# Optimization experiments

Hardware: AMD Instinct MI355X
Metric: run time of the kernel (lower is better)

Reference implementation:

```python
import jax, jax.numpy as jnp
import numpy as np

HID = 2048; S = 2048; NH = 16
Q_LORA = 1536; KV_LORA = 512
D_NOPE = 128; D_ROPE = 64; D_V = 128
D_QK = D_NOPE + D_ROPE  # 192
EPS = 1e-6


def setup_inputs() -> dict:
    key = jax.random.key(0)
    ks = jax.random.split(key, 8)
    hidden_states = jax.random.normal(ks[0], (1, S, HID), dtype=jnp.float32)
    # real RoPE tables, HF layout: cos/sin = concat(freqs, freqs) along last dim
    inv_freq = 1.0 / (10000.0 ** (np.arange(0, D_ROPE, 2, dtype=np.float32) / D_ROPE))
    t = np.arange(S, dtype=np.float32)
    freqs = np.outer(t, inv_freq)  # [S, D_ROPE//2]
    emb = np.concatenate([freqs, freqs], axis=-1)  # [S, D_ROPE]
    cos = jnp.asarray(np.cos(emb))[None]  # [1, S, D_ROPE]
    sin = jnp.asarray(np.sin(emb))[None]
    def lin(k, fan_in, fan_out):
        return jax.random.normal(k, (fan_in, fan_out), dtype=jnp.float32) / np.sqrt(fan_in)
    return {
        'hidden_states': hidden_states, 'cos': cos, 'sin': sin,
        'w_qa': lin(ks[1], HID, Q_LORA),
        'g_qa': jnp.ones((Q_LORA,), jnp.float32),
        'w_qb': lin(ks[2], Q_LORA, NH * D_QK),
        'w_kva': lin(ks[3], HID, KV_LORA + D_ROPE),
        'g_kva': jnp.ones((KV_LORA,), jnp.float32),
        'w_kvb': lin(ks[4], KV_LORA, NH * (D_NOPE + D_V)),
        'w_o': lin(ks[5], NH * D_V, HID),
    }


def _rmsnorm(x, g):
    var = jnp.mean(x * x, axis=-1, keepdims=True)
    return x * jax.lax.rsqrt(var + EPS) * g


def _deinterleave(x):
    # view (..., d//2, 2) -> transpose -> reshape: even-index dims first, then odd
    b, h, s, d = x.shape
    return x.reshape(b, h, s, d // 2, 2).transpose(0, 1, 2, 4, 3).reshape(b, h, s, d)


def _rotate_half(x):
    x1, x2 = jnp.split(x, 2, axis=-1)
    return jnp.concatenate([-x2, x1], axis=-1)


def _apply_rope(q, k, cos, sin):
    cos = cos[:, None]  # [B,1,S,D]
    sin = sin[:, None]
    q = _deinterleave(q)
    k = _deinterleave(k)
    q_emb = q * cos + _rotate_half(q) * sin
    k_emb = k * cos + _rotate_half(k) * sin
    return q_emb, k_emb


def reference(hidden_states, cos, sin, w_qa, g_qa, w_qb, w_kva, g_kva, w_kvb, w_o):
    bsz, q_len, _ = hidden_states.shape
    # low-rank Q projection
    q = _rmsnorm(hidden_states @ w_qa, g_qa) @ w_qb  # [B,S,NH*D_QK]
    q = q.reshape(bsz, q_len, NH, D_QK).transpose(0, 2, 1, 3)  # [B,NH,S,D_QK]
    q_nope, q_pe = q[..., :D_NOPE], q[..., D_NOPE:]
    # compressed KV + shared rope key
    ckv = hidden_states @ w_kva  # [B,S,KV_LORA+D_ROPE]
    compressed_kv, k_pe = ckv[..., :KV_LORA], ckv[..., KV_LORA:]
    k_pe = k_pe.reshape(bsz, q_len, 1, D_ROPE).transpose(0, 2, 1, 3)  # [B,1,S,D_ROPE]
    kv = (_rmsnorm(compressed_kv, g_kva) @ w_kvb).reshape(bsz, q_len, NH, D_NOPE + D_V).transpose(0, 2, 1, 3)
    k_nope, value_states = kv[..., :D_NOPE], kv[..., D_NOPE:]
    # interleaved RoPE
    q_pe, k_pe = _apply_rope(q_pe, k_pe, cos, sin)
    query_states = jnp.concatenate([q_nope, q_pe], axis=-1)  # [B,NH,S,D_QK]
    key_states = jnp.concatenate([k_nope, jnp.broadcast_to(k_pe, (bsz, NH, q_len, D_ROPE))], axis=-1)
    # causal attention with MLA softmax scale
    scale = D_QK ** (-0.5)
    scores = jnp.einsum('bhqd,bhkd->bhqk', query_states, key_states) * scale
    mask = jnp.tril(jnp.ones((q_len, q_len), dtype=bool))
    scores = jnp.where(mask, scores, jnp.finfo(scores.dtype).min)
    probs = jax.nn.softmax(scores, axis=-1)
    attn = jnp.einsum('bhqk,bhkd->bhqd', probs, value_states)  # [B,NH,S,D_V]
    attn = attn.transpose(0, 2, 1, 3).reshape(bsz, q_len, NH * D_V)
    return attn @ w_o
```

## Files before the change

### kernel.cpp

```cpp
#include <hip/hip_runtime.h>
#include <hip/hip_bf16.h>

#define S_LEN 2048
#define HID_D 2048
#define NHEAD 16
#define QLORA 1536
#define KVLORA 512
#define DNOPE 128
#define DROPE 64
#define DV 128
#define DQK 192
#define CKV_PAD 640

#define KS_SH (64 * 192)
#define VS_SH (128 * 64)
#define BUF_SH (KS_SH + VS_SH)

typedef __hip_bfloat16 bf16;
typedef __attribute__((ext_vector_type(8))) short short8;
typedef __attribute__((ext_vector_type(4))) short s16x4;
typedef __attribute__((ext_vector_type(4))) float f32x4;

__device__ __forceinline__ float ldE(const float* p) { return *p; }
__device__ __forceinline__ float ldE(const bf16* p) { return __bfloat162float(*p); }
__device__ __forceinline__ void stE(float* p, float v) { *p = v; }
__device__ __forceinline__ void stE(bf16* p, float v) { *p = __float2bfloat16(v); }

__device__ __forceinline__ short bf16bits(float v) {
    __hip_bfloat16 h = __float2bfloat16(v);
    return *reinterpret_cast<short*>(&h);
}

__device__ __forceinline__ float b2f(short s) {
    union { short s; bf16 h; } u;
    u.s = s;
    return __bfloat162float(u.h);
}

__device__ __forceinline__ f32x4 mfma16(short8 a, short8 b, f32x4 c) {
    return __builtin_amdgcn_mfma_f32_16x16x32_bf16(a, b, c, 0, 0, 0);
}

__device__ __forceinline__ void gload16(const void* g, void* l) {
    __builtin_amdgcn_global_load_lds(
        (const __attribute__((address_space(1))) unsigned int*)g,
        (__attribute__((address_space(3))) unsigned int*)l, 16, 0, 0);
}

__global__ void detect_kernel(const void* hidden, int* flag) {
    __shared__ int red[256];
    const int tid = threadIdx.x;
    const bf16* hb = (const bf16*)hidden;
    float a = fabsf(__bfloat162float(hb[tid]));
    red[tid] = (!(a < 64.f) || (a != 0.f && a < 1e-30f)) ? 1 : 0;
    __syncthreads();
    for (int o = 128; o > 0; o >>= 1) {
        if (tid < o) red[tid] += red[tid + o];
        __syncthreads();
    }
    if (tid == 0) *flag = (red[0] > 16) ? 1 : 0;
}

__global__ void convert_kernel(const void* in, bf16* out, int n8, const int* flag) {
    int i = blockIdx.x * 256 + threadIdx.x;
    if (i >= n8) return;
    size_t off = (size_t)i * 8;
    short8 o;
    if (*flag) {
        const float* f = (const float*)in + off;
#pragma unroll
        for (int j = 0; j < 8; ++j) o[j] = bf16bits(f[j]);
    } else {
        o = *(const short8*)((const short*)in + off);
    }
    *(short8*)((short*)out + off) = o;
}

__global__ void transpose_kernel(const void* in, bf16* out, int K, int N, int Npad,
                                 const int* flag) {
    __shared__ __align__(16) short Ts[64][80];
    const int tid = threadIdx.x;
    const int n0 = blockIdx.x * 64, k0 = blockIdx.y * 64;
    const bool inb = n0 < N;
    const int fp32 = *flag;
    const int kl = tid >> 4;
    const int nl = (tid & 15) * 4;
#pragma unroll
    for (int p = 0; p < 4; ++p) {
        int k = kl + p * 16;
        float v[4] = {0.f, 0.f, 0.f, 0.f};
        if (inb) {
            if (fp32) {
                const float4 f = *(const float4*)((const float*)in + (size_t)(k0 + k) * N + n0 + nl);
                v[0] = f.x; v[1] = f.y; v[2] = f.z; v[3] = f.w;
            } else {
                const bf16* bp = (const bf16*)in + (size_t)(k0 + k) * N + n0 + nl;
#pragma unroll
                for (int i = 0; i < 4; ++i) v[i] = __bfloat162float(bp[i]);
            }
        }
#pragma unroll
        for (int i = 0; i < 4; ++i) Ts[nl + i][k] = bf16bits(v[i]);
    }
    __syncthreads();
    const int nr = tid >> 2;
    const int kq = (tid & 3) * 16;
    short* op = (short*)out + (size_t)(n0 + nr) * K + k0 + kq;
    *(short8*)op = *(short8*)&Ts[nr][kq];
    *(short8*)(op + 8) = *(short8*)&Ts[nr][kq + 8];
}

template <int MODE, typename TC>
__device__ void mgemm_body(const bf16* __restrict__ A, const bf16* __restrict__ Bt,
                           TC* __restrict__ C, int M, int N, int K,
                           bf16* __restrict__ Kn, bf16* __restrict__ Vt) {
    __shared__ __align__(16) short As[128 * 32];
    __shared__ __align__(16) short Bs[128 * 32];
    const int tid = threadIdx.x;
    const int w = tid >> 6, lane = tid & 63;
    const int lg = lane >> 4, ln = lane & 15;
    const int wm = w >> 1, wn = w & 1;
    const int m0 = blockIdx.y * 128, n0 = blockIdx.x * 128;

    const int c0 = w * 128 + lane, c1 = c0 + 64;
    const int r0 = c0 >> 2, kq0 = (c0 & 3) ^ ((r0 >> 1) & 3);
    const int r1 = c1 >> 2, kq1 = (c1 & 3) ^ ((r1 >> 1) & 3);
    const bf16* aP0 = A + (size_t)(m0 + r0) * K + kq0 * 8;
    const bf16* aP1 = A + (size_t)(m0 + r1) * K + kq1 * 8;
    const bf16* bP0 = Bt + (size_t)(n0 + r0) * K + kq0 * 8;
    const bf16* bP1 = Bt + (size_t)(n0 + r1) * K + kq1 * 8;
    short* aL0 = As + (size_t)(w * 128) * 8;
    short* aL1 = As + (size_t)(w * 128 + 64) * 8;
    short* bL0 = Bs + (size_t)(w * 128) * 8;
    short* bL1 = Bs + (size_t)(w * 128 + 64) * 8;

    const int sx = lg ^ ((ln >> 1) & 3);
    int aoff[4], boff[4];
#pragma unroll
    for (int i = 0; i < 4; ++i) {
        aoff[i] = (wm * 64 + i * 16 + ln) * 32 + sx * 8;
        boff[i] = (wn * 64 + i * 16 + ln) * 32 + sx * 8;
    }

    f32x4 acc[4][4];
#pragma unroll
    for (int i = 0; i < 4; ++i)
#pragma unroll
        for (int j = 0; j < 4; ++j) acc[i][j] = (f32x4){0.f, 0.f, 0.f, 0.f};

    for (int k0 = 0; k0 < K; k0 += 32) {
        __syncthreads();
        gload16(aP0 + k0, aL0);
        gload16(aP1 + k0, aL1);
        gload16(bP0 + k0, bL0);
        gload16(bP1 + k0, bL1);
        __syncthreads();
        short8 af[4], bfr[4];
#pragma unroll
        for (int i = 0; i < 4; ++i) af[i] = *(const short8*)&As[aoff[i]];
#pragma unroll
        for (int j = 0; j < 4; ++j) bfr[j] = *(const short8*)&Bs[boff[j]];
#pragma unroll
        for (int i = 0; i < 4; ++i)
#pragma unroll
            for (int j = 0; j < 4; ++j) acc[i][j] = mfma16(af[i], bfr[j], acc[i][j]);
    }
    if constexpr (MODE == 2) {
#pragma unroll
        for (int i = 0; i < 4; ++i)
#pragma unroll
            for (int j = 0; j < 4; ++j) {
                const int col = n0 + wn * 64 + j * 16 + ln;
                const int row = m0 + wm * 64 + i * 16 + lg * 4;
                const int h = col >> 8, d = col & 255;
                if (d < DNOPE) {
                    bf16* cp = Kn + (size_t)row * (NHEAD * DNOPE) + h * DNOPE + d;
#pragma unroll
                    for (int r = 0; r < 4; ++r)
                        cp[(size_t)r * (NHEAD * DNOPE)] = __float2bfloat16(acc[i][j][r]);
                } else {
                    s16x4 pk;
#pragma unroll
                    for (int r = 0; r < 4; ++r) pk[r] = bf16bits(acc[i][j][r]);
                    *(s16x4*)(Vt + (size_t)(h * DV + (d - DNOPE)) * S_LEN + row) = pk;
                }
            }
    } else {
#pragma unroll
        for (int i = 0; i < 4; ++i)
#pragma unroll
            for (int j = 0; j < 4; ++j) {
                TC* cp = C + (size_t)(m0 + wm * 64 + i * 16 + lg * 4) * N + n0 + wn * 64 + j * 16 + ln;
#pragma unroll
                for (int r = 0; r < 4; ++r)
                    stE(cp + (size_t)r * N, acc[i][j][r]);
            }
    }
}

template <int MODE>
__global__ __launch_bounds__(256, 2)
void mgemm_kernel(const bf16* A, const bf16* Bt, void* C, int M, int N, int K,
                  const int* flag, bf16* Kn, bf16* Vt) {
    if (MODE == 1 && *flag) mgemm_body<1, float>(A, Bt, (float*)C, M, N, K, nullptr, nullptr);
    else if (MODE == 2)     mgemm_body<2, bf16>(A, Bt, (bf16*)C, M, N, K, Kn, Vt);
    else                    mgemm_body<0, bf16>(A, Bt, (bf16*)C, M, N, K, nullptr, nullptr);
}

template <typename TG>
__device__ void rmsnorm_body(const bf16* __restrict__ x, const TG* __restrict__ g,
                             bf16* __restrict__ y, int len, int xstride, int ystride) {
    const int s = blockIdx.x;
    const int tid = threadIdx.x;
    const bf16* xr = x + (size_t)s * xstride;
    float ss = 0.f;
    for (int i = tid; i < len; i += 256) {
        float v = __bfloat162float(xr[i]);
        ss += v * v;
    }
    __shared__ float red[256];
    red[tid] = ss;
    __syncthreads();
    for (int o = 128; o > 0; o >>= 1) {
        if (tid < o) red[tid] += red[tid + o];
        __syncthreads();
    }
    const float scale = rsqrtf(red[0] / (float)len + 1e-6f);
    bf16* yr = y + (size_t)s * ystride;
    for (int i = tid; i < len; i += 256)
        yr[i] = __float2bfloat16(__bfloat162float(xr[i]) * scale * ldE(&g[i]));
}

__global__ void rmsnorm_kernel(const bf16* x, const void* g, bf16* y,
                               int len, int xstride, int ystride, const int* flag) {
    if (*flag) rmsnorm_body<float>(x, (const float*)g, y, len, xstride, ystride);
    else       rmsnorm_body<bf16>(x, (const bf16*)g, y, len, xstride, ystride);
}

template <typename TG>
__device__ void rope_body(bf16* __restrict__ q, const bf16* __restrict__ ckv,
                          bf16* __restrict__ kpe, const TG* __restrict__ cosb,
                          const TG* __restrict__ sinb) {
    const int s = blockIdx.x;
    const int tid = threadIdx.x;
    float x0 = 0.f, x1 = 0.f, c = 0.f, sn = 0.f;
    bf16* qbase = nullptr;
    int p = 0;
    const bool isq = tid < 512;
    const bool active = tid < 544;
    if (active) {
        if (isq) {
            const int h = tid >> 5;
            p = tid & 31;
            qbase = q + (size_t)s * (NHEAD * DQK) + h * DQK + DNOPE;
            x0 = __bfloat162float(qbase[2 * p]);
            x1 = __bfloat162float(qbase[2 * p + 1]);
        } else {
            p = tid - 512;
            const bf16* kb = ckv + (size_t)s * CKV_PAD + KVLORA;
            x0 = __bfloat162float(kb[2 * p]);
            x1 = __bfloat162float(kb[2 * p + 1]);
        }
        c = ldE(&cosb[s * 64 + p]);
        sn = ldE(&sinb[s * 64 + p]);
    }
    __syncthreads();
    if (active) {
        if (isq) {
            qbase[p] = __float2bfloat16(x0 * c - x1 * sn);
            qbase[p + 32] = __float2bfloat16(x1 * c + x0 * sn);
        } else {
            kpe[s * 64 + p] = __float2bfloat16(x0 * c - x1 * sn);
            kpe[s * 64 + p + 32] = __float2bfloat16(x1 * c + x0 * sn);
        }
    }
}

__global__ void rope_kernel(bf16* q, const bf16* ckv, bf16* kpe,
                            const void* cosb, const void* sinb, const int* flag) {
    if (*flag) rope_body<float>(q, ckv, kpe, (const float*)cosb, (const float*)sinb);
    else       rope_body<bf16>(q, ckv, kpe, (const bf16*)cosb, (const bf16*)sinb);
}

__global__ __launch_bounds__(256, 2)
void fattn_kernel(const bf16* __restrict__ q, const bf16* __restrict__ kn,
                  const bf16* __restrict__ vt, const bf16* __restrict__ kpe,
                  bf16* __restrict__ attn, bf16* __restrict__ Opart, float* __restrict__ ml) {
    const int nf = blockIdx.x;
    const int xcd = nf & 7;
    const int j = nf >> 3;
    const int bx = j & 31;
    const int h = (j >> 5) * 8 + xcd;
    int qt, part, nparts;
    if (bx < 15)      { qt = 15 - bx / 3;        part = bx % 3;        nparts = 3; }
    else if (bx < 27) { qt = 10 - (bx - 15) / 2; part = (bx - 15) & 1; nparts = 2; }
    else              { qt = 31 - bx;            part = 0;             nparts = 1; }
    const int nt = 2 * qt + 2;
    const int bsz = nt / nparts, rr = nt % nparts;
    const int t0 = part * bsz + (part < rr ? part : rr);
    const int t1 = t0 + bsz + (part < rr ? 1 : 0);
    const int q0 = qt * 128;

    const int tid = threadIdx.x;
    const int w = tid >> 6;
    const int l = tid & 63;
    const int lg = l >> 4;
    const int ln = l & 15;

    __shared__ __align__(16) short KV[2][BUF_SH];

    int offK[6], sK[6];
    bool isn[6];
#pragma unroll
    for (int p = 0; p < 6; ++p) {
        const int cid = tid + p * 256;
        const int row = cid / 24;
        const int cpos = cid % 24;
        const int c = (cpos & 24) | ((cpos & 7) ^ (row & 7));
        if (c < 16) {
            offK[p] = row * (NHEAD * DNOPE) + h * DNOPE + c * 8;
            sK[p] = NHEAD * DNOPE;
            isn[p] = true;
        } else {
            offK[p] = row * DROPE + (c - 16) * 8;
            sK[p] = DROPE;
            isn[p] = false;
        }
    }
    int offV[4];
#pragma unroll
    for (int p = 0; p < 4; ++p) {
        const int cid = tid + p * 256;
        const int row = cid >> 3;
        const int cc = (cid & 7) ^ (row & 7);
        offV[p] = (h * DV + row) * S_LEN + cc * 8;
    }

    short8 qf[2][6];
#pragma unroll
    for (int i = 0; i < 2; ++i) {
        const short* qrow =
            (const short*)(q + (size_t)(q0 + i * 64 + w * 16 + ln) * (NHEAD * DQK) + h * DQK);
#pragma unroll
        for (int ks = 0; ks < 6; ++ks)
            qf[i][ks] = *(const short8*)(qrow + ks * 32 + lg * 8);
    }

    f32x4 O[2][8];
#pragma unroll
    for (int i = 0; i < 2; ++i)
#pragma unroll
        for (int ct = 0; ct < 8; ++ct) O[i][ct] = (f32x4){0.f, 0.f, 0.f, 0.f};
    float m_[2][4], l_[2][4];
#pragma unroll
    for (int i = 0; i < 2; ++i)
#pragma unroll
        for (int r = 0; r < 4; ++r) { m_[i][r] = -1e30f; l_[i][r] = 0.f; }
    const float scale = 0.07216878364870322f;

    {
        const int k0 = t0 * 64;
#pragma unroll
        for (int p = 0; p < 6; ++p) {
            const bf16* sp = (isn[p] ? kn : kpe) + (size_t)offK[p] + (size_t)k0 * sK[p];
            gload16(sp, &KV[0][0] + (w + 4 * p) * 512);
        }
#pragma unroll
        for (int p = 0; p < 4; ++p)
            gload16(vt + (size_t)offV[p] + k0, &KV[0][KS_SH] + (w + 4 * p) * 512);
    }

    for (int t = t0; t < t1; ++t) {
        const int cur = (t - t0) & 1;
        short* Ks = &KV[cur][0];
        short* Vs = &KV[cur][KS_SH];
        if (t + 1 < t1) {
            const int k0n = (t + 1) * 64;
            short* KsN = &KV[cur ^ 1][0];
            short* VsN = &KV[cur ^ 1][KS_SH];
#pragma unroll
            for (int p = 0; p < 6; ++p) {
                const bf16* sp = (isn[p] ? kn : kpe) + (size_t)offK[p] + (size_t)k0n * sK[p];
                gload16(sp, KsN + (w + 4 * p) * 512);
            }
#pragma unroll
            for (int p = 0; p < 4; ++p)
                gload16(vt + (size_t)offV[p] + k0n, VsN + (w + 4 * p) * 512);
            asm volatile("s_waitcnt vmcnt(10)" ::: "memory");
        } else {
            asm volatile("s_waitcnt vmcnt(0)" ::: "memory");
        }
        __builtin_amdgcn_s_barrier();

        const int k0 = t * 64;
        f32x4 S[2][4];
#pragma unroll
        for (int i = 0; i < 2; ++i)
#pragma unroll
            for (int c = 0; c < 4; ++c) S[i][c] = (f32x4){0.f, 0.f, 0.f, 0.f};
        __builtin_amdgcn_s_setprio(1);
#pragma unroll
        for (int ks = 0; ks < 6; ++ks) {
            const int kch = ks * 4 + lg;
#pragma unroll
            for (int c = 0; c < 4; ++c) {
                short8 kf = *(const short8*)&Ks[(size_t)(c * 16 + ln) * 192 +
                                               (size_t)(kch ^ (ln & 7)) * 8];
                S[0][c] = mfma16(qf[0][ks], kf, S[0][c]);
                S[1][c] = mfma16(qf[1][ks], kf, S[1][c]);
            }
        }
        __builtin_amdgcn_s_setprio(0);

        const int d0 = k0 - q0;
#pragma unroll
        for (int i = 0; i < 2; ++i)
#pragma unroll
            for (int c = 0; c < 4; ++c)
#pragma unroll
                for (int r = 0; r < 4; ++r) {
                    float v = S[i][c][r] * scale;
                    if (d0 > -64 &&
                        (d0 + c * 16 + ln) > (i * 64 + w * 16 + lg * 4 + r)) v = -1e30f;
                    S[i][c][r] = v;
                }

        float alpha[2][4];
#pragma unroll
        for (int i = 0; i < 2; ++i)
#pragma unroll
            for (int r = 0; r < 4; ++r) {
                float mx = fmaxf(fmaxf(S[i][0][r], S[i][1][r]), fmaxf(S[i][2][r], S[i][3][r]));
#pragma unroll
                for (int d = 1; d < 16; d <<= 1) mx = fmaxf(mx, __shfl_xor(mx, d));
                float mn = fmaxf(m_[i][r], mx);
                alpha[i][r] = __expf(m_[i][r] - mn);
                m_[i][r] = mn;
                float rs = 0.f;
#pragma unroll
                for (int c = 0; c < 4; ++c) {
                    float p = __expf(S[i][c][r] - mn);
                    S[i][c][r] = p;
                    rs += p;
                }
#pragma unroll
                for (int d = 1; d < 16; d <<= 1) rs += __shfl_xor(rs, d);
                l_[i][r] = l_[i][r] * alpha[i][r] + rs;
            }
#pragma unroll
        for (int i = 0; i < 2; ++i)
#pragma unroll
            for (int ct = 0; ct < 8; ++ct)
#pragma unroll
                for (int r = 0; r < 4; ++r) O[i][ct][r] *= alpha[i][r];

        __builtin_amdgcn_s_barrier();
        short* Pb = Ks;
#pragma unroll
        for (int i = 0; i < 2; ++i)
#pragma unroll
            for (int c = 0; c < 4; ++c)
#pragma unroll
                for (int r = 0; r < 4; ++r)
                    Pb[(size_t)(i * 64 + w * 16 + lg * 4 + r) * 70 + c * 16 + ln] =
                        bf16bits(S[i][c][r]);

        __builtin_amdgcn_s_setprio(1);
#pragma unroll
        for (int ks = 0; ks < 2; ++ks) {
            short8 pf0 = *(const short8*)&Pb[(size_t)(w * 16 + ln) * 70 + ks * 32 + lg * 8];
            short8 pf1 = *(const short8*)&Pb[(size_t)(64 + w * 16 + ln) * 70 + ks * 32 + lg * 8];
#pragma unroll
            for (int ct = 0; ct < 8; ++ct) {
                short8 vf = *(const short8*)&Vs[(size_t)(ct * 16 + ln) * 64 +
                                               (size_t)((ks * 4 + lg) ^ (ln & 7)) * 8];
                O[0][ct] = mfma16(pf0, vf, O[0][ct]);
                O[1][ct] = mfma16(pf1, vf, O[1][ct]);
            }
        }
        __builtin_amdgcn_s_setprio(0);
        __builtin_amdgcn_s_barrier();
    }

    if (nparts == 1) {
#pragma unroll
        for (int i = 0; i < 2; ++i)
#pragma unroll
            for (int r = 0; r < 4; ++r) {
                float inv = 1.f / l_[i][r];
                bf16* orow = attn + (size_t)(q0 + i * 64 + w * 16 + lg * 4 + r) * (NHEAD * DV) +
                             h * DV;
#pragma unroll
                for (int ct = 0; ct < 8; ++ct)
                    orow[ct * 16 + ln] = __float2bfloat16(O[i][ct][r] * inv);
            }
    } else {
        const int mlslot = h * 27 + (qt <= 10 ? (qt - 5) * 2 + part : 12 + (qt - 11) * 3 + part);
        float* mlp = ml + (size_t)mlslot * 128 * 2;
        if (part == 0) {
#pragma unroll
            for (int i = 0; i < 2; ++i)
#pragma unroll
                for (int r = 0; r < 4; ++r) {
                    const int rowb = i * 64 + w * 16 + lg * 4 + r;
                    bf16* orow = attn + (size_t)(q0 + rowb) * (NHEAD * DV) + h * DV;
#pragma unroll
                    for (int ct = 0; ct < 8; ++ct)
                        orow[ct * 16 + ln] = __float2bfloat16(O[i][ct][r]);
                    if (ln == 0) {
                        mlp[rowb * 2] = m_[i][r];
                        mlp[rowb * 2 + 1] = l_[i][r];
                    }
                }
        } else {
            const int oslot = h * 16 + (qt <= 10 ? (qt - 5) : 6 + (qt - 11) * 2 + (part - 1));
            bf16* op = Opart + (size_t)oslot * 128 * DV;
#pragma unroll
            for (int i = 0; i < 2; ++i)
#pragma unroll
                for (int r = 0; r < 4; ++r) {
                    const int rowb = i * 64 + w * 16 + lg * 4 + r;
#pragma unroll
                    for (int ct = 0; ct < 8; ++ct)
                        op[(size_t)rowb * DV + ct * 16 + ln] = __float2bfloat16(O[i][ct][r]);
                    if (ln == 0) {
                        mlp[rowb * 2] = m_[i][r];
                        mlp[rowb * 2 + 1] = l_[i][r];
                    }
                }
        }
    }
}

__global__ void reduce_kernel(const bf16* __restrict__ Opart, const float* __restrict__ ml,
                              bf16* __restrict__ attn) {
    const int qq = blockIdx.x;
    const int h = blockIdx.y;
    const int qt = 5 + qq;
    const int np = (qt <= 10) ? 2 : 3;
    const int q0 = qt * 128;
    const int tid = threadIdx.x;
    const int row = tid >> 1;
    const int dh = (tid & 1) * 64;
    float mp[3], lp[3], f[3];
    float mm = -1e30f;
    for (int p = 0; p < np; ++p) {
        const int msl = h * 27 + (qt <= 10 ? (qt - 5) * 2 + p : 12 + (qt - 11) * 3 + p);
        mp[p] = ml[((size_t)msl * 128 + row) * 2];
        lp[p] = ml[((size_t)msl * 128 + row) * 2 + 1];
        mm = fmaxf(mm, mp[p]);
    }
    float denom = 0.f;
    for (int p = 0; p < np; ++p) {
        f[p] = __expf(mp[p] - mm);
        denom += f[p] * lp[p];
    }
    const float inv = 1.f / denom;
    const int os1 = h * 16 + (qt <= 10 ? (qt - 5) : 6 + (qt - 11) * 2);
    bf16* arow = attn + (size_t)(q0 + row) * (NHEAD * DV) + h * DV + dh;
    const bf16* o1 = Opart + ((size_t)os1 * 128 + row) * DV + dh;
    const bf16* o2 = o1 + (size_t)128 * DV;
#pragma unroll
    for (int jc = 0; jc < 8; ++jc) {
        short8 a = *(const short8*)(arow + jc * 8);
        short8 b1 = *(const short8*)(o1 + jc * 8);
        short8 b2 = (np == 3) ? *(const short8*)(o2 + jc * 8) : b1;
        short8 o;
#pragma unroll
        for (int e = 0; e < 8; ++e) {
            float v = f[0] * b2f(a[e]) + f[1] * b2f(b1[e]);
            if (np == 3) v += f[2] * b2f(b2[e]);
            o[e] = bf16bits(v * inv);
        }
        *(short8*)(arow + jc * 8) = o;
    }
}

extern "C" void kernel_launch(void* const* d_in, const int* in_sizes, int n_in,
                              void* d_out, int out_size, void* d_ws, size_t ws_size,
                              hipStream_t stream) {
    const void* hidden = d_in[0];
    const void* cosb   = d_in[1];
    const void* sinb   = d_in[2];
    const void* w_qa   = d_in[3];
    const void* g_qa   = d_in[4];
    const void* w_qb   = d_in[5];
    const void* w_kva  = d_in[6];
    const void* g_kva  = d_in[7];
    const void* w_kvb  = d_in[8];
    const void* w_o    = d_in[9];

    bf16* ws = (bf16*)d_ws;
    bf16* q_a  = ws;
    bf16* ckv  = q_a + (size_t)S_LEN * QLORA;
    bf16* ckvn = ckv + (size_t)S_LEN * CKV_PAD;
    bf16* q    = ckvn + (size_t)S_LEN * KVLORA;
    bf16* kn   = q + (size_t)S_LEN * NHEAD * DQK;
    bf16* vtb  = kn + (size_t)S_LEN * NHEAD * DNOPE;
    bf16* kpe  = vtb + (size_t)NHEAD * DV * S_LEN;
    bf16* hbf  = kpe + (size_t)S_LEN * DROPE;
    int* flag  = (int*)(hbf + (size_t)S_LEN * HID_D);
    bf16* attn = ws;
    float* ml  = (float*)(ws + (size_t)S_LEN * HID_D);
    bf16* Opart = hbf;
    bf16* W01  = kn;
    bf16* W23  = q_a;
    bf16* W4   = q;

    detect_kernel<<<1, 256, 0, stream>>>(hidden, flag);
    convert_kernel<<<(S_LEN * HID_D / 8 + 255) / 256, 256, 0, stream>>>(
        hidden, hbf, S_LEN * HID_D / 8, flag);

    transpose_kernel<<<dim3(QLORA / 64, HID_D / 64), 256, 0, stream>>>(
        w_qa, W01, HID_D, QLORA, QLORA, flag);
    mgemm_kernel<0><<<dim3(QLORA / 128, S_LEN / 128), 256, 0, stream>>>(
        hbf, W01, q_a, S_LEN, QLORA, HID_D, flag, nullptr, nullptr);
    rmsnorm_kernel<<<S_LEN, 256, 0, stream>>>(q_a, g_qa, q_a, QLORA, QLORA, QLORA, flag);
    transpose_kernel<<<dim3(NHEAD * DQK / 64, QLORA / 64), 256, 0, stream>>>(
        w_qb, W01, QLORA, NHEAD * DQK, NHEAD * DQK, flag);
    mgemm_kernel<0><<<dim3(NHEAD * DQK / 128, S_LEN / 128), 256, 0, stream>>>(
        q_a, W01, q, S_LEN, NHEAD * DQK, QLORA, flag, nullptr, nullptr);
    transpose_kernel<<<dim3(CKV_PAD / 64, HID_D / 64), 256, 0, stream>>>(
        w_kva, W23, HID_D, KVLORA + DROPE, CKV_PAD, flag);
    mgemm_kernel<0><<<dim3(CKV_PAD / 128, S_LEN / 128), 256, 0, stream>>>(
        hbf, W23, ckv, S_LEN, CKV_PAD, HID_D, flag, nullptr, nullptr);
    rmsnorm_kernel<<<S_LEN, 256, 0, stream>>>(ckv, g_kva, ckvn, KVLORA, CKV_PAD, KVLORA, flag);
    transpose_kernel<<<dim3(NHEAD * (DNOPE + DV) / 64, KVLORA / 64), 256, 0, stream>>>(
        w_kvb, W23, KVLORA, NHEAD * (DNOPE + DV), NHEAD * (DNOPE + DV), flag);
    mgemm_kernel<2><<<dim3(NHEAD * (DNOPE + DV) / 128, S_LEN / 128), 256, 0, stream>>>(
        ckvn, W23, kn, S_LEN, NHEAD * (DNOPE + DV), KVLORA, flag, kn, vtb);
    rope_kernel<<<S_LEN, 576, 0, stream>>>(q, ckv, kpe, cosb, sinb, flag);
    fattn_kernel<<<dim3(512), 256, 0, stream>>>(q, kn, vtb, kpe, attn, Opart, ml);
    reduce_kernel<<<dim3(11, NHEAD), 256, 0, stream>>>(Opart, ml, attn);
    transpose_kernel<<<dim3(HID_D / 64, HID_D / 64), 256, 0, stream>>>(
        w_o, W4, HID_D, HID_D, HID_D, flag);
    mgemm_kernel<1><<<dim3(HID_D / 128, S_LEN / 128), 256, 0, stream>>>(
        attn, W4, d_out, S_LEN, HID_D, HID_D, flag, nullptr, nullptr);
}
```

Before: 408.4 us.

## Merge q_a and kv_a projections into one GEMM and deepen GEMM K-tile

Concatenates the transposed w_qa and w_kva weights so a single GEMM over the hidden states produces both the q low-rank and compressed-KV outputs, with fused transpose and RMSNorm launches for both branches. The GEMM gains explicit leading dimensions and a K step of 64 instead of 32, with an 8-way XOR swizzle, halving the number of barrier pairs per tile. This removes several launches and the CKV padding and improves per-barrier MFMA density. In exchange LDS use per block doubles, which may limit occupancy, and workspace aliasing becomes more intricate.

```diff
diff --git a/kernel.cpp b/kernel.cpp
--- a/kernel.cpp
+++ b/kernel.cpp
@@ -10,7 +10,7 @@
 #define DROPE 64
 #define DV 128
 #define DQK 192
-#define CKV_PAD 640
+#define NCAT 2176
 
 #define KS_SH (64 * 192)
 #define VS_SH (128 * 64)
@@ -76,6 +76,39 @@
     *(short8*)((short*)out + off) = o;
 }
 
+template <int KDIM>
+__device__ void transpose_tile(const void* in, bf16* out, int N, int n0, int k0,
+                               int roff, int fp32) {
+    __shared__ __align__(16) short Ts[64][80];
+    const int tid = threadIdx.x;
+    const bool inb = n0 < N;
+    const int kl = tid >> 4;
+    const int nl = (tid & 15) * 4;
+#pragma unroll
+    for (int p = 0; p < 4; ++p) {
+        int k = kl + p * 16;
+        float v[4] = {0.f, 0.f, 0.f, 0.f};
+        if (inb) {
+            if (fp32) {
+                const float4 f = *(const float4*)((const float*)in + (size_t)(k0 + k) * N + n0 + nl);
+                v[0] = f.x; v[1] = f.y; v[2] = f.z; v[3] = f.w;
+            } else {
+                const bf16* bp = (const bf16*)in + (size_t)(k0 + k) * N + n0 + nl;
+#pragma unroll
+                for (int i = 0; i < 4; ++i) v[i] = __bfloat162float(bp[i]);
+            }
+        }
+#pragma unroll
+        for (int i = 0; i < 4; ++i) Ts[nl + i][k] = bf16bits(v[i]);
+    }
+    __syncthreads();
+    const int nr = tid >> 2;
+    const int kq = (tid & 3) * 16;
+    short* op = (short*)out + (size_t)(roff + n0 + nr) * KDIM + k0 + kq;
+    *(short8*)op = *(short8*)&Ts[nr][kq];
+    *(short8*)(op + 8) = *(short8*)&Ts[nr][kq + 8];
+}
+
 __global__ void transpose_kernel(const void* in, bf16* out, int K, int N, int Npad,
                                  const int* flag) {
     __shared__ __align__(16) short Ts[64][80];
@@ -110,37 +143,48 @@
     *(short8*)(op + 8) = *(short8*)&Ts[nr][kq + 8];
 }
 
+__global__ void transpose2_kernel(const void* inA, const void* inB, bf16* out,
+                                  const int* flag) {
+    const int bx = blockIdx.x;
+    const int k0 = blockIdx.y * 64;
+    const int fp32 = *flag;
+    if (bx < 24) transpose_tile<HID_D>(inA, out, QLORA, bx * 64, k0, 0, fp32);
+    else         transpose_tile<HID_D>(inB, out, KVLORA + DROPE, (bx - 24) * 64, k0, QLORA, fp32);
+}
+
 template <int MODE, typename TC>
-__device__ void mgemm_body(const bf16* __restrict__ A, const bf16* __restrict__ Bt,
-                           TC* __restrict__ C, int M, int N, int K,
+__device__ void mgemm_body(const bf16* __restrict__ A, int lda,
+                           const bf16* __restrict__ Bt, int ldb,
+                           TC* __restrict__ C, int ldc, int K,
                            bf16* __restrict__ Kn, bf16* __restrict__ Vt) {
-    __shared__ __align__(16) short As[128 * 32];
-    __shared__ __align__(16) short Bs[128 * 32];
+    __shared__ __align__(16) short As[128 * 64];
+    __shared__ __align__(16) short Bs[128 * 64];
     const int tid = threadIdx.x;
     const int w = tid >> 6, lane = tid & 63;
     const int lg = lane >> 4, ln = lane & 15;
     const int wm = w >> 1, wn = w & 1;
     const int m0 = blockIdx.y * 128, n0 = blockIdx.x * 128;
 
-    const int c0 = w * 128 + lane, c1 = c0 + 64;
-    const int r0 = c0 >> 2, kq0 = (c0 & 3) ^ ((r0 >> 1) & 3);
-    const int r1 = c1 >> 2, kq1 = (c1 & 3) ^ ((r1 >> 1) & 3);
-    const bf16* aP0 = A + (size_t)(m0 + r0) * K + kq0 * 8;
-    const bf16* aP1 = A + (size_t)(m0 + r1) * K + kq1 * 8;
-    const bf16* bP0 = Bt + (size_t)(n0 + r0) * K + kq0 * 8;
-    const bf16* bP1 = Bt + (size_t)(n0 + r1) * K + kq1 * 8;
-    short* aL0 = As + (size_t)(w * 128) * 8;
-    short* aL1 = As + (size_t)(w * 128 + 64) * 8;
-    short* bL0 = Bs + (size_t)(w * 128) * 8;
-    short* bL1 = Bs + (size_t)(w * 128 + 64) * 8;
-
-    const int sx = lg ^ ((ln >> 1) & 3);
-    int aoff[4], boff[4];
-#pragma unroll
-    for (int i = 0; i < 4; ++i) {
-        aoff[i] = (wm * 64 + i * 16 + ln) * 32 + sx * 8;
-        boff[i] = (wn * 64 + i * 16 + ln) * 32 + sx * 8;
-    }
+    const bf16* aP[4];
+    const bf16* bP[4];
+#pragma unroll
+    for (int p = 0; p < 4; ++p) {
+        const int cid = tid + p * 256;
+        const int row = cid >> 3, cpos = cid & 7;
+        const int c = cpos ^ (row & 7);
+        aP[p] = A + (size_t)(m0 + row) * lda + c * 8;
+        bP[p] = Bt + (size_t)(n0 + row) * ldb + c * 8;
+    }
+    int aoff[2][4], boff[2][4];
+#pragma unroll
+    for (int hk = 0; hk < 2; ++hk)
+#pragma unroll
+        for (int i = 0; i < 4; ++i) {
+            const int ra = wm * 64 + i * 16 + ln;
+            const int rb = wn * 64 + i * 16 + ln;
+            aoff[hk][i] = ra * 64 + ((hk * 4 + lg) ^ (ra & 7)) * 8;
+            boff[hk][i] = rb * 64 + ((hk * 4 + lg) ^ (rb & 7)) * 8;
+        }
 
     f32x4 acc[4][4];
 #pragma unroll
@@ -148,22 +192,26 @@
 #pragma unroll
         for (int j = 0; j < 4; ++j) acc[i][j] = (f32x4){0.f, 0.f, 0.f, 0.f};
 
-    for (int k0 = 0; k0 < K; k0 += 32) {
+    for (int k0 = 0; k0 < K; k0 += 64) {
         __syncthreads();
-        gload16(aP0 + k0, aL0);
-        gload16(aP1 + k0, aL1);
-        gload16(bP0 + k0, bL0);
-        gload16(bP1 + k0, bL1);
+#pragma unroll
+        for (int p = 0; p < 4; ++p) {
+            gload16(aP[p] + k0, As + (w + 4 * p) * 512);
+            gload16(bP[p] + k0, Bs + (w + 4 * p) * 512);
+        }
         __syncthreads();
-        short8 af[4], bfr[4];
-#pragma unroll
-        for (int i = 0; i < 4; ++i) af[i] = *(const short8*)&As[aoff[i]];
-#pragma unroll
-        for (int j = 0; j < 4; ++j) bfr[j] = *(const short8*)&Bs[boff[j]];
-#pragma unroll
-        for (int i = 0; i < 4; ++i)
-#pragma unroll
-            for (int j = 0; j < 4; ++j) acc[i][j] = mfma16(af[i], bfr[j], acc[i][j]);
+#pragma unroll
+        for (int hk = 0; hk < 2; ++hk) {
+            short8 af[4], bfr[4];
+#pragma unroll
+            for (int i = 0; i < 4; ++i) af[i] = *(const short8*)&As[aoff[hk][i]];
+#pragma unroll
+            for (int j = 0; j < 4; ++j) bfr[j] = *(const short8*)&Bs[boff[hk][j]];
+#pragma unroll
+            for (int i = 0; i < 4; ++i)
+#pragma unroll
+                for (int j = 0; j < 4; ++j) acc[i][j] = mfma16(af[i], bfr[j], acc[i][j]);
+        }
     }
     if constexpr (MODE == 2) {
 #pragma unroll
@@ -190,29 +238,31 @@
         for (int i = 0; i < 4; ++i)
 #pragma unroll
             for (int j = 0; j < 4; ++j) {
-                TC* cp = C + (size_t)(m0 + wm * 64 + i * 16 + lg * 4) * N + n0 + wn * 64 + j * 16 + ln;
+                TC* cp = C + (size_t)(m0 + wm * 64 + i * 16 + lg * 4) * ldc + n0 + wn * 64 +
+                         j * 16 + ln;
 #pragma unroll
                 for (int r = 0; r < 4; ++r)
-                    stE(cp + (size_t)r * N, acc[i][j][r]);
+                    stE(cp + (size_t)r * ldc, acc[i][j][r]);
             }
     }
 }
 
 template <int MODE>
 __global__ __launch_bounds__(256, 2)
-void mgemm_kernel(const bf16* A, const bf16* Bt, void* C, int M, int N, int K,
-                  const int* flag, bf16* Kn, bf16* Vt) {
-    if (MODE == 1 && *flag) mgemm_body<1, float>(A, Bt, (float*)C, M, N, K, nullptr, nullptr);
-    else if (MODE == 2)     mgemm_body<2, bf16>(A, Bt, (bf16*)C, M, N, K, Kn, Vt);
-    else                    mgemm_body<0, bf16>(A, Bt, (bf16*)C, M, N, K, nullptr, nullptr);
+void mgemm_kernel(const bf16* A, int lda, const bf16* Bt, int ldb, void* C, int ldc,
+                  int K, const int* flag, bf16* Kn, bf16* Vt) {
+    if (MODE == 1 && *flag)
+        mgemm_body<1, float>(A, lda, Bt, ldb, (float*)C, ldc, K, nullptr, nullptr);
+    else if (MODE == 2)
+        mgemm_body<2, bf16>(A, lda, Bt, ldb, (bf16*)C, ldc, K, Kn, Vt);
+    else
+        mgemm_body<0, bf16>(A, lda, Bt, ldb, (bf16*)C, ldc, K, nullptr, nullptr);
 }
 
 template <typename TG>
-__device__ void rmsnorm_body(const bf16* __restrict__ x, const TG* __restrict__ g,
-                             bf16* __restrict__ y, int len, int xstride, int ystride) {
-    const int s = blockIdx.x;
+__device__ void rmsnorm_row(const bf16* __restrict__ xr, const TG* __restrict__ g,
+                            bf16* __restrict__ yr, int len) {
     const int tid = threadIdx.x;
-    const bf16* xr = x + (size_t)s * xstride;
     float ss = 0.f;
     for (int i = tid; i < len; i += 256) {
         float v = __bfloat162float(xr[i]);
@@ -226,15 +276,32 @@
         __syncthreads();
     }
     const float scale = rsqrtf(red[0] / (float)len + 1e-6f);
-    bf16* yr = y + (size_t)s * ystride;
     for (int i = tid; i < len; i += 256)
         yr[i] = __float2bfloat16(__bfloat162float(xr[i]) * scale * ldE(&g[i]));
 }
 
-__global__ void rmsnorm_kernel(const bf16* x, const void* g, bf16* y,
-                               int len, int xstride, int ystride, const int* flag) {
-    if (*flag) rmsnorm_body<float>(x, (const float*)g, y, len, xstride, ystride);
-    else       rmsnorm_body<bf16>(x, (const bf16*)g, y, len, xstride, ystride);
+__global__ void rmsnorm2_kernel(bf16* qk, const void* g_qa, const void* g_kva,
+                                bf16* ckvn, const int* flag) {
+    const int bid = blockIdx.x;
+    if (*flag) {
+        if (bid < S_LEN)
+            rmsnorm_row<float>(qk + (size_t)bid * NCAT, (const float*)g_qa,
+                               qk + (size_t)bid * NCAT, QLORA);
+        else {
+            const int s = bid - S_LEN;
+            rmsnorm_row<float>(qk + (size_t)s * NCAT + QLORA, (const float*)g_kva,
+                               ckvn + (size_t)s * KVLORA, KVLORA);
+        }
+    } else {
+        if (bid < S_LEN)
+            rmsnorm_row<bf16>(qk + (size_t)bid * NCAT, (const bf16*)g_qa,
+                              qk + (size_t)bid * NCAT, QLORA);
+        else {
+            const int s = bid - S_LEN;
+            rmsnorm_row<bf16>(qk + (size_t)s * NCAT + QLORA, (const bf16*)g_kva,
+                              ckvn + (size_t)s * KVLORA, KVLORA);
+        }
+    }
 }
 
 template <typename TG>
@@ -257,7 +324,7 @@
             x1 = __bfloat162float(qbase[2 * p + 1]);
         } else {
             p = tid - 512;
-            const bf16* kb = ckv + (size_t)s * CKV_PAD + KVLORA;
+            const bf16* kb = ckv + (size_t)s * NCAT + KVLORA;
             x0 = __bfloat162float(kb[2 * p]);
             x1 = __bfloat162float(kb[2 * p + 1]);
         }
@@ -591,9 +658,8 @@
     const void* w_o    = d_in[9];
 
     bf16* ws = (bf16*)d_ws;
-    bf16* q_a  = ws;
-    bf16* ckv  = q_a + (size_t)S_LEN * QLORA;
-    bf16* ckvn = ckv + (size_t)S_LEN * CKV_PAD;
+    bf16* qk   = ws;
+    bf16* ckvn = qk + (size_t)S_LEN * NCAT;
     bf16* q    = ckvn + (size_t)S_LEN * KVLORA;
     bf16* kn   = q + (size_t)S_LEN * NHEAD * DQK;
     bf16* vtb  = kn + (size_t)S_LEN * NHEAD * DNOPE;
@@ -603,37 +669,32 @@
     bf16* attn = ws;
     float* ml  = (float*)(ws + (size_t)S_LEN * HID_D);
     bf16* Opart = hbf;
-    bf16* W01  = kn;
-    bf16* W23  = q_a;
-    bf16* W4   = q;
+    bf16* BtCat = kn;
+    bf16* wqbT  = kn;
+    bf16* wkvbT = hbf;
+    bf16* W4    = q;
 
     detect_kernel<<<1, 256, 0, stream>>>(hidden, flag);
     convert_kernel<<<(S_LEN * HID_D / 8 + 255) / 256, 256, 0, stream>>>(
         hidden, hbf, S_LEN * HID_D / 8, flag);
 
-    transpose_kernel<<<dim3(QLORA / 64, HID_D / 64), 256, 0, stream>>>(
-        w_qa, W01, HID_D, QLORA, QLORA, flag);
-    mgemm_kernel<0><<<dim3(QLORA / 128, S_LEN / 128), 256, 0, stream>>>(
-        hbf, W01, q_a, S_LEN, QLORA, HID_D, flag, nullptr, nullptr);
-    rmsnorm_kernel<<<S_LEN, 256, 0, stream>>>(q_a, g_qa, q_a, QLORA, QLORA, QLORA, flag);
+    transpose2_kernel<<<dim3(34, HID_D / 64), 256, 0, stream>>>(w_qa, w_kva, BtCat, flag);
+    mgemm_kernel<0><<<dim3(NCAT / 128, S_LEN / 128), 256, 0, stream>>>(
+        hbf, HID_D, BtCat, HID_D, qk, NCAT, HID_D, flag, nullptr, nullptr);
+    rmsnorm2_kernel<<<2 * S_LEN, 256, 0, stream>>>(qk, g_qa, g_kva, ckvn, flag);
     transpose_kernel<<<dim3(NHEAD * DQK / 64, QLORA / 64), 256, 0, stream>>>(
-        w_qb, W01, QLORA, NHEAD * DQK, NHEAD * DQK, flag);
+        w_qb, wqbT, QLORA, NHEAD * DQK, NHEAD * DQK, flag);
     mgemm_kernel<0><<<dim3(NHEAD * DQK / 128, S_LEN / 128), 256, 0, stream>>>(
-        q_a, W01, q, S_LEN, NHEAD * DQK, QLORA, flag, nullptr, nullptr);
-    transpose_kernel<<<dim3(CKV_PAD / 64, HID_D / 64), 256, 0, stream>>>(
-        w_kva, W23, HID_D, KVLORA + DROPE, CKV_PAD, flag);
-    mgemm_kernel<0><<<dim3(CKV_PAD / 128, S_LEN / 128), 256, 0, stream>>>(
-        hbf, W23, ckv, S_LEN, CKV_PAD, HID_D, flag, nullptr, nullptr);
-    rmsnorm_kernel<<<S_LEN, 256, 0, stream>>>(ckv, g_kva, ckvn, KVLORA, CKV_PAD, KVLORA, flag);
+        qk, NCAT, wqbT, QLORA, q, NHEAD * DQK, QLORA, flag, nullptr, nullptr);
     transpose_kernel<<<dim3(NHEAD * (DNOPE + DV) / 64, KVLORA / 64), 256, 0, stream>>>(
-        w_kvb, W23, KVLORA, NHEAD * (DNOPE + DV), NHEAD * (DNOPE + DV), flag);
+        w_kvb, wkvbT, KVLORA, NHEAD * (DNOPE + DV), NHEAD * (DNOPE + DV), flag);
     mgemm_kernel<2><<<dim3(NHEAD * (DNOPE + DV) / 128, S_LEN / 128), 256, 0, stream>>>(
-        ckvn, W23, kn, S_LEN, NHEAD * (DNOPE + DV), KVLORA, flag, kn, vtb);
-    rope_kernel<<<S_LEN, 576, 0, stream>>>(q, ckv, kpe, cosb, sinb, flag);
+        ckvn, KVLORA, wkvbT, KVLORA, kn, NHEAD * (DNOPE + DV), KVLORA, flag, kn, vtb);
+    rope_kernel<<<S_LEN, 576, 0, stream>>>(q, qk + QLORA, kpe, cosb, sinb, flag);
     fattn_kernel<<<dim3(512), 256, 0, stream>>>(q, kn, vtb, kpe, attn, Opart, ml);
     reduce_kernel<<<dim3(11, NHEAD), 256, 0, stream>>>(Opart, ml, attn);
     transpose_kernel<<<dim3(HID_D / 64, HID_D / 64), 256, 0, stream>>>(
         w_o, W4, HID_D, HID_D, HID_D, flag);
     mgemm_kernel<1><<<dim3(HID_D / 128, S_LEN / 128), 256, 0, stream>>>(
-        attn, W4, d_out, S_LEN, HID_D, HID_D, flag, nullptr, nullptr);
-}
+        attn, NHEAD * DV, W4, HID_D, d_out, HID_D, HID_D, flag, nullptr, nullptr);
+}
```

New measurement: 346.6 us. 15.1% less time.
